# Optimization experiments

Measured on AMD Instinct MI355X. Metric: run time of the kernel, lower is better.

The kernel has to match this reference:

```python
import jax, jax.numpy as jnp
import numpy as np

N_LEVELS = 16
F_PER_LEVEL = 2
T = 1 << 19  # hashmap size per level
BASE_RES = 16
DST_RES = 4096
B = float(np.exp(np.log(DST_RES / BASE_RES) / (N_LEVELS - 1)))  # per-level scale
MOVING_STEP = 1.0 / 4096.0
AABB_MIN = -1.5
AABB_MAX = 1.5
GEO_FEAT_DIM = 15
CORNERS = np.array([[i, j, k] for i in (0, 1) for j in (0, 1) for k in (0, 1)], dtype=np.int32)  # [8,3]
PRIMES = np.array([1, 2654435761, 805459861], dtype=np.uint32)


def mlp(h, Ws):
    # tcnn FullyFusedMLP: bias-free linear layers, ReLU hidden, linear output
    for W in Ws[:-1]:
        h = jax.nn.relu(h @ W)
    return h @ Ws[-1]


def freq_encode(x, n_freqs):
    # tcnn Frequency encoding: sin/cos(2^f * pi * x) per dim/freq; [N,D] -> [N, D*n_freqs*2]
    f = (2.0 ** jnp.arange(n_freqs, dtype=jnp.float32)) * jnp.pi
    xf = x[..., None] * f  # [N, D, nf]
    return jnp.concatenate([jnp.sin(xf), jnp.cos(xf)], axis=-1).reshape(x.shape[0], -1)


def sh_encode_deg4(d):
    # real spherical harmonics, degree 4 (16 coeffs), unit direction input
    x, y, z = d[..., 0], d[..., 1], d[..., 2]
    xy, yz, xz = x * y, y * z, x * z
    x2, y2, z2 = x * x, y * y, z * z
    return jnp.stack([
        0.28209479177387814 * jnp.ones_like(x),
        -0.48860251190291987 * y,
        0.48860251190291987 * z,
        -0.48860251190291987 * x,
        1.0925484305920792 * xy,
        -1.0925484305920792 * yz,
        0.94617469575755997 * z2 - 0.31539156525251999,
        -1.0925484305920792 * xz,
        0.54627421529603959 * (x2 - y2),
        0.59004358992664352 * y * (y2 - 3.0 * x2),
        2.8906114426405538 * xy * z,
        0.45704579946446572 * y * (1.0 - 5.0 * z2),
        0.3731763325901154 * z * (5.0 * z2 - 3.0),
        0.45704579946446572 * x * (1.0 - 5.0 * z2),
        1.4453057213202769 * z * (x2 - y2),
        0.59004358992664352 * x * (3.0 * y2 - x2),
    ], axis=-1)  # [N,16]


def hash_encode(x, tables):
    # x: [N,3] in [0,1]; tables: [L, T, F]. Multi-res grid w/ trilinear interp;
    # dense indexing for small levels, spatial hashing for large ones (tcnn semantics).
    outs = []
    for l in range(N_LEVELS):
        scale = BASE_RES * (B ** l) - 1.0
        res = int(np.ceil(scale)) + 1
        pos = x * scale + 0.5
        pos0 = jnp.floor(pos)
        frac = pos - pos0
        c = pos0.astype(jnp.int32)[:, None, :] + CORNERS[None]  # [N,8,3]
        if res ** 3 <= T:
            idx = c[..., 0] + res * (c[..., 1] + res * c[..., 2])
        else:
            cu = c.astype(jnp.uint32)
            idx = (cu[..., 0] * PRIMES[0]) ^ (cu[..., 1] * PRIMES[1]) ^ (cu[..., 2] * PRIMES[2])
            idx = (idx % np.uint32(T)).astype(jnp.int32)
        feats = tables[l][idx]  # [N,8,F] gather
        w = jnp.prod(jnp.where(CORNERS[None] == 1, frac[:, None, :], 1.0 - frac[:, None, :]), axis=-1)  # [N,8]
        outs.append(jnp.einsum('ncf,nc->nf', feats, w))
    return jnp.concatenate(outs, axis=-1)  # [N, L*F]


def _w(k, fan_in, fan_out):
    return jax.random.normal(k, (fan_in, fan_out), jnp.float32) / np.sqrt(fan_in)


def setup_inputs() -> dict:
    key = jax.random.key(0)
    ks = jax.random.split(key, 12)
    N = 524288
    positions = jax.random.uniform(ks[0], (N, 3), jnp.float32, -1.2, 1.2)
    t = jax.random.uniform(ks[1], (N, 1), jnp.float32)
    directions = jax.random.normal(ks[2], (N, 3), jnp.float32)
    tables = jax.random.uniform(ks[3], (N_LEVELS, T, F_PER_LEVEL), jnp.float32, -1e-4, 1e-4)
    return {
        'positions': positions, 't': t, 'directions': directions, 'tables': tables,
        'w_wrap0': _w(ks[4], 32, 64), 'w_wrap1': _w(ks[5], 64, 64), 'w_wrap2': _w(ks[6], 64, 3),
        'w_base0': _w(ks[7], 32, 64), 'w_base1': _w(ks[8], 64, 1 + GEO_FEAT_DIM),
        'w_head0': _w(ks[9], 16 + GEO_FEAT_DIM, 64), 'w_head1': _w(ks[10], 64, 64), 'w_head2': _w(ks[11], 64, 3),
    }


def reference(positions, t, directions, tables,
              w_wrap0, w_wrap1, w_wrap2, w_base0, w_base1,
              w_head0, w_head1, w_head2):
    # query_move: frequency-encode (x,t), tiny MLP -> offsets, scaled by MOVING_STEP
    enc = freq_encode(jnp.concatenate([positions, t], axis=-1), 4)  # [N,32]
    offsets = mlp(enc, [w_wrap0, w_wrap1, w_wrap2])  # [N,3]
    x_move = positions + offsets * MOVING_STEP
    # normalize to aabb unit cube
    xn = (x_move - AABB_MIN) / (AABB_MAX - AABB_MIN)
    selector = jnp.all((xn > 0.0) & (xn < 1.0), axis=-1)
    hash_feat = hash_encode(xn, tables)  # [N,32]
    base = mlp(hash_feat, [w_base0, w_base1])  # [N,16]
    density = jnp.exp(base[:, :1] - 1.0) * selector[:, None].astype(base.dtype)  # trunc_exp(x-1)
    geo = base[:, 1:]
    dirs = directions / jnp.linalg.norm(directions, axis=-1, keepdims=True)
    sh = sh_encode_deg4(dirs)  # [N,16]
    rgb = jax.nn.sigmoid(mlp(jnp.concatenate([sh, geo], axis=-1), [w_head0, w_head1, w_head2]))
    return jnp.concatenate([rgb, density], axis=-1)  # [N,4] = (rgb, density)
```

## Files before the change

kernel.cpp:

```cpp
#include <hip/hip_runtime.h>
#include <math.h>

#define TPB   128
#define HTPB  256
#define HPTS  4
#define CHUNK 32
#define LDW   68
constexpr int  N_LVL = 16;
constexpr unsigned TBL = 1u << 19;
constexpr float MOVE_STEP = 1.0f / 4096.0f;

typedef __attribute__((ext_vector_type(8))) short short8;
typedef __attribute__((ext_vector_type(4))) float f32x4;
typedef __attribute__((ext_vector_type(4), aligned(8))) float f32x4u;

struct LevelParams { float scale[N_LVL]; int res[N_LVL]; int dense[N_LVL]; };

enum { C_W0 = 0, C_W1 = 4, C_W2 = 12, C_B0 = 14, C_B1 = 18, C_H0 = 20, C_H1 = 24, C_H2 = 32, C_TOT = 34 };

struct LayerDesc { const float* W; int K; int N; int ksteps; int ntiles; int cbase; };
struct AllLayers { LayerDesc L[8]; };

__device__ __forceinline__ unsigned short f2bf(float x) {
    unsigned int u = __float_as_uint(x);
    u += 0x7FFFu + ((u >> 16) & 1u);
    return (unsigned short)(u >> 16);
}
__device__ __forceinline__ float bf2f(unsigned short h) {
    return __uint_as_float(((unsigned int)h) << 16);
}
__device__ __forceinline__ unsigned pk(unsigned short a, unsigned short b) {
    return (unsigned)a | ((unsigned)b << 16);
}
__device__ __forceinline__ unsigned sel4(uint4 w, unsigned i) {
    const unsigned lo = (i & 1u) ? w.y : w.x;
    const unsigned hi = (i & 1u) ? w.w : w.z;
    return (i & 2u) ? hi : lo;
}

__device__ __forceinline__ unsigned cvt_pk_bf16(float a, float b) {
    unsigned r;
    asm("v_cvt_pk_bf16_f32 %0, %1, %2" : "=v"(r) : "v"(a), "v"(b));
    return r;
}
__device__ __forceinline__ void split_pair(float a, float b, unsigned& hp, unsigned& lp) {
    hp = cvt_pk_bf16(a, b);
    const float ha = __uint_as_float(hp << 16);
    const float hb = __uint_as_float(hp & 0xffff0000u);
    lp = cvt_pk_bf16(a - ha, b - hb);
}

__global__ __launch_bounds__(256) void k_prep(AllLayers al, unsigned short* __restrict__ wfrag)
{
    const LayerDesc d = al.L[blockIdx.x];
    const int total = d.ksteps * d.ntiles * 64;
    for (int slot = threadIdx.x; slot < total; slot += 256) {
        const int lane = slot & 63;
        const int c = slot >> 6;
        const int s = c / d.ntiles;
        const int t = c - s * d.ntiles;
        short8 hv, lv;
#pragma unroll
        for (int j = 0; j < 8; ++j) {
            const int k = s * 32 + ((lane >> 4) << 3) + j;
            const int n = t * 16 + (lane & 15);
            const float w = (k < d.K && n < d.N) ? d.W[k * d.N + n] : 0.f;
            const unsigned short hi = f2bf(w);
            const unsigned short lo = f2bf(w - bf2f(hi));
            hv[j] = (short)hi;
            lv[j] = (short)lo;
        }
        short8* b8 = reinterpret_cast<short8*>(wfrag + (size_t)(d.cbase + c) * 1024);
        b8[lane]      = hv;
        b8[64 + lane] = lv;
    }
}

__global__ __launch_bounds__(256) void k_tab16(
    const float* __restrict__ g_tab, unsigned* __restrict__ tab16,
    int n_dense, int n_hashed)
{
    const size_t total_pairs = (size_t)n_hashed * (TBL / 2);
    const size_t gstride = (size_t)gridDim.x * 256;
    const float* __restrict__ src = g_tab + (size_t)n_dense * (TBL * 2);
    for (size_t i = (size_t)blockIdx.x * 256 + threadIdx.x; i < total_pairs; i += gstride) {
        const f32x4 v = reinterpret_cast<const f32x4*>(src)[i];
        uint2 o;
        o.x = pk(f2bf(v[0]), f2bf(v[1]));
        o.y = pk(f2bf(v[2]), f2bf(v[3]));
        reinterpret_cast<uint2*>(tab16)[i] = o;
    }
}

template<int KSTEPS, int NTILES, int TERMS, bool RELU>
__device__ __forceinline__ void wave_layer(float* X,
                                           const unsigned short* __restrict__ wfrag, int cbase,
                                           int wrow, int lane)
{
    f32x4 acc[2][NTILES];
#pragma unroll
    for (int ms = 0; ms < 2; ++ms)
#pragma unroll
        for (int t = 0; t < NTILES; ++t) acc[ms][t] = f32x4{0.f, 0.f, 0.f, 0.f};
    const int r15 = lane & 15, q = lane >> 4;
    const short8* wf8 = reinterpret_cast<const short8*>(wfrag) + (size_t)cbase * 128;
#pragma unroll
    for (int s = 0; s < KSTEPS; ++s) {
        short8 ah[2], al[2];
#pragma unroll
        for (int ms = 0; ms < 2; ++ms) {
            const float* xp = X + (size_t)(wrow + ms * 16 + r15) * LDW + s * 32 + q * 8;
            const f32x4 x0 = reinterpret_cast<const f32x4*>(xp)[0];
            const f32x4 x1 = reinterpret_cast<const f32x4*>(xp)[1];
            union { unsigned u[4]; short8 s8; } uh, ul;
            if (TERMS == 3) {
                split_pair(x0[0], x0[1], uh.u[0], ul.u[0]);
                split_pair(x0[2], x0[3], uh.u[1], ul.u[1]);
                split_pair(x1[0], x1[1], uh.u[2], ul.u[2]);
                split_pair(x1[2], x1[3], uh.u[3], ul.u[3]);
                al[ms] = ul.s8;
            } else {
                uh.u[0] = cvt_pk_bf16(x0[0], x0[1]);
                uh.u[1] = cvt_pk_bf16(x0[2], x0[3]);
                uh.u[2] = cvt_pk_bf16(x1[0], x1[1]);
                uh.u[3] = cvt_pk_bf16(x1[2], x1[3]);
            }
            ah[ms] = uh.s8;
        }
#pragma unroll
        for (int t = 0; t < NTILES; ++t) {
            const short8* cp = wf8 + (size_t)(s * NTILES + t) * 128;
            const short8 bh = cp[lane];
            short8 bl;
            if (TERMS == 3) bl = cp[64 + lane];
#pragma unroll
            for (int ms = 0; ms < 2; ++ms) {
                acc[ms][t] = __builtin_amdgcn_mfma_f32_16x16x32_bf16(ah[ms], bh, acc[ms][t], 0, 0, 0);
                if (TERMS == 3) {
                    acc[ms][t] = __builtin_amdgcn_mfma_f32_16x16x32_bf16(al[ms], bh, acc[ms][t], 0, 0, 0);
                    acc[ms][t] = __builtin_amdgcn_mfma_f32_16x16x32_bf16(ah[ms], bl, acc[ms][t], 0, 0, 0);
                }
            }
        }
    }
#pragma unroll
    for (int ms = 0; ms < 2; ++ms)
#pragma unroll
        for (int t = 0; t < NTILES; ++t)
#pragma unroll
            for (int r = 0; r < 4; ++r) {
                float v = acc[ms][t][r];
                if (RELU) v = fmaxf(v, 0.f);
                X[(size_t)(wrow + ms * 16 + q * 4 + r) * LDW + t * 16 + r15] = v;
            }
}

__global__ __launch_bounds__(256, 4) void k_warp_mfma(
    const float* __restrict__ g_pos, const float* __restrict__ g_t,
    const float* __restrict__ g_tab,
    const unsigned short* __restrict__ wfrag,
    float* __restrict__ xn4,
    unsigned* __restrict__ featp, size_t stride, int N, int n_dense, LevelParams lp)
{
    __shared__ float buf[128 * LDW];
    const int tid = threadIdx.x;
    const int base = blockIdx.x * 128;
    const int p = tid & 127;
    const int pn = min(base + p, N - 1);
    const float PI_F = 3.14159265358979323846f;

    {
        const int dpair = tid >> 7;
        float v0, v1;
        if (dpair == 0) { v0 = g_pos[3 * pn + 0]; v1 = g_pos[3 * pn + 1]; }
        else            { v0 = g_pos[3 * pn + 2]; v1 = g_t[pn]; }
#pragma unroll
        for (int e = 0; e < 2; ++e) {
            const float x = e ? v1 : v0;
            const int d = dpair * 2 + e;
            f32x4 sv, cv;
#pragma unroll
            for (int k = 0; k < 4; ++k) {
                const float a = x * (PI_F * (float)(1 << k));
                sv[k] = __sinf(a);
                cv[k] = __cosf(a);
            }
            *reinterpret_cast<f32x4*>(&buf[(size_t)p * LDW + d * 8])     = sv;
            *reinterpret_cast<f32x4*>(&buf[(size_t)p * LDW + d * 8 + 4]) = cv;
        }
    }
    __syncthreads();
    const int lane = tid & 63, wrow = (tid >> 6) * 32;
    wave_layer<1, 4, 1, true >(buf, wfrag, C_W0, wrow, lane);
    wave_layer<2, 4, 1, true >(buf, wfrag, C_W1, wrow, lane);
    wave_layer<2, 1, 1, false>(buf, wfrag, C_W2, wrow, lane);

    const int prow = wrow + (lane & 31);
    const int sub  = lane >> 5;
    const int n = base + prow;
    const int pn2 = min(n, N - 1);
    const float ox = buf[(size_t)prow * LDW + 0];
    const float oy = buf[(size_t)prow * LDW + 1];
    const float oz = buf[(size_t)prow * LDW + 2];
    const float xnv[3] = { (g_pos[3 * pn2 + 0] + ox * MOVE_STEP + 1.5f) / 3.0f,
                           (g_pos[3 * pn2 + 1] + oy * MOVE_STEP + 1.5f) / 3.0f,
                           (g_pos[3 * pn2 + 2] + oz * MOVE_STEP + 1.5f) / 3.0f };
    if (sub == 0 && n < N) {
        reinterpret_cast<f32x4*>(xn4)[n] = f32x4{ xnv[0], xnv[1], xnv[2], 0.f };
    }

    const int dmid = min(3, n_dense);
    const int l0 = sub ? dmid : 0;
    const int l1 = sub ? n_dense : dmid;
    for (int l = l0; l < l1; ++l) {
        const float scale = lp.scale[l];
        const int res = lp.res[l];
        float fr[3]; int c0[3];
#pragma unroll
        for (int d = 0; d < 3; ++d) {
            const float pp = xnv[d] * scale + 0.5f;
            const float fl = floorf(pp);
            fr[d] = pp - fl;
            c0[d] = (int)fl;
        }
        const float* __restrict__ tbl = g_tab + (size_t)l * (size_t)(TBL * 2);
        f32x4u v[4];
#pragma unroll
        for (int pc = 0; pc < 4; ++pc) {
            const int cj = pc >> 1, ck = pc & 1;
            const int idx = c0[0] + res * ((c0[1] + cj) + res * (c0[2] + ck));
            v[pc] = *reinterpret_cast<const f32x4u*>(tbl + (size_t)idx * 2);
        }
        float f0 = 0.f, f1 = 0.f;
        const float wx0 = 1.f - fr[0], wx1 = fr[0];
#pragma unroll
        for (int pc = 0; pc < 4; ++pc) {
            const int cj = pc >> 1, ck = pc & 1;
            const float wyz = (cj ? fr[1] : 1.f - fr[1]) * (ck ? fr[2] : 1.f - fr[2]);
            f0 = fmaf(wx0 * wyz, v[pc][0], f0);
            f1 = fmaf(wx0 * wyz, v[pc][1], f1);
            f0 = fmaf(wx1 * wyz, v[pc][2], f0);
            f1 = fmaf(wx1 * wyz, v[pc][3], f1);
        }
        if (n < N) {
            __builtin_nontemporal_store(pk(f2bf(f0), f2bf(f1)), &featp[(size_t)l * stride + n]);
        }
    }
}

__global__ __launch_bounds__(HTPB) void k_hash_all16(
    const unsigned* __restrict__ tab16,
    const float* __restrict__ xn4,
    unsigned* __restrict__ featp, size_t stride, int N, int n_dense, LevelParams lp)
{
    const int l = n_dense + blockIdx.y;
    const float scale = lp.scale[l];
    const unsigned* __restrict__ tbl = tab16 + (size_t)blockIdx.y * TBL;
    unsigned* __restrict__ op = featp + (size_t)l * stride;

    const int base = blockIdx.x * (HTPB * HPTS) + threadIdx.x;

#pragma unroll
    for (int b = 0; b < HPTS; b += 2) {
        int nn[2]; bool av[2];
        f32x4 xs[2];
#pragma unroll
        for (int j = 0; j < 2; ++j) {
            nn[j] = base + (b + j) * HTPB;
            av[j] = nn[j] < N;
            xs[j] = reinterpret_cast<const f32x4*>(xn4)[av[j] ? nn[j] : 0];
        }

        float frx[2];
        float wyz[2][4];
        uint4 w4[2][4];
        unsigned vodd[2][4] = {};
        unsigned a3p[2], mm[2];
        bool far_[2];
#pragma unroll
        for (int j = 0; j < 2; ++j) {
            int c0[3]; float fr[3];
#pragma unroll
            for (int d = 0; d < 3; ++d) {
                const float pp = xs[j][d] * scale + 0.5f;
                const float fl = floorf(pp);
                fr[d] = pp - fl;
                c0[d] = (int)fl;
            }
            frx[j] = fr[0];
            const unsigned ux  = (unsigned)c0[0];
            const unsigned ry0 = (unsigned)c0[1] * 2654435761u;
            const unsigned ry1 = (unsigned)(c0[1] + 1) * 2654435761u;
            const unsigned rz0 = (unsigned)c0[2] * 805459861u;
            const unsigned rz1 = (unsigned)(c0[2] + 1) * 805459861u;
            mm[j]  = ux ^ (ux + 1u);
            far_[j] = mm[j] > 3u;
            const float wy0 = 1.f - fr[1], wy1 = fr[1];
            const float wz0 = 1.f - fr[2], wz1 = fr[2];
            wyz[j][0] = wy0 * wz0; wyz[j][1] = wy0 * wz1;
            wyz[j][2] = wy1 * wz0; wyz[j][3] = wy1 * wz1;
            const unsigned rr[4] = { ry0 ^ rz0, ry0 ^ rz1, ry1 ^ rz0, ry1 ^ rz1 };
            unsigned a3 = 0;
#pragma unroll
            for (int pc = 0; pc < 4; ++pc) {
                const unsigned iA = (ux ^ rr[pc]) & (TBL - 1u);
                a3 |= (iA & 3u) << (2 * pc);
                w4[j][pc] = *reinterpret_cast<const uint4*>(tbl + (iA & ~3u));
            }
            a3p[j] = a3;
            if (far_[j]) {
#pragma unroll
                for (int pc = 0; pc < 4; ++pc) {
                    const unsigned iB = ((ux + 1u) ^ rr[pc]) & (TBL - 1u);
                    vodd[j][pc] = tbl[iB];
                }
            }
        }

#pragma unroll
        for (int j = 0; j < 2; ++j) {
            float f0 = 0.f, f1 = 0.f;
            const float wx0 = 1.f - frx[j], wx1 = frx[j];
#pragma unroll
            for (int pc = 0; pc < 4; ++pc) {
                const unsigned a3 = (a3p[j] >> (2 * pc)) & 3u;
                const unsigned vA = sel4(w4[j][pc], a3);
                const unsigned vB = far_[j] ? vodd[j][pc] : sel4(w4[j][pc], a3 ^ mm[j]);
                const float wA = wx0 * wyz[j][pc];
                const float wB = wx1 * wyz[j][pc];
                f0 = fmaf(wA, bf2f((unsigned short)(vA & 0xffffu)), f0);
                f1 = fmaf(wA, bf2f((unsigned short)(vA >> 16)), f1);
                f0 = fmaf(wB, bf2f((unsigned short)(vB & 0xffffu)), f0);
                f1 = fmaf(wB, bf2f((unsigned short)(vB >> 16)), f1);
            }
            if (av[j]) __builtin_nontemporal_store(pk(f2bf(f0), f2bf(f1)), &op[nn[j]]);
        }
    }
}

__global__ __launch_bounds__(256, 4) void k_final_mfma(
    const unsigned* __restrict__ featp, size_t stride,
    const float* __restrict__ xn4,
    const float* __restrict__ g_dir,
    const unsigned short* __restrict__ wfrag,
    float* __restrict__ g_out, int N)
{
    __shared__ float buf[128 * LDW];
    const int tid = threadIdx.x;
    const int base = blockIdx.x * 128;
    const int p = tid & 127;
    const int pn = min(base + p, N - 1);
    const int g = tid >> 7;

#pragma unroll
    for (int j = 0; j < 8; ++j) {
        const int l = g * 8 + j;
        const unsigned v = __builtin_nontemporal_load(&featp[(size_t)l * stride + pn]);
        buf[(size_t)p * LDW + 2 * l]     = bf2f((unsigned short)(v & 0xffffu));
        buf[(size_t)p * LDW + 2 * l + 1] = bf2f((unsigned short)(v >> 16));
    }
    __syncthreads();

    const int lane = tid & 63, wrow = (tid >> 6) * 32;
    wave_layer<1, 4, 1, true >(buf, wfrag, C_B0, wrow, lane);
    wave_layer<2, 1, 1, false>(buf, wfrag, C_B1, wrow, lane);
    __syncthreads();

    float density = 0.f;
    if (tid < 128) {
        float bb[16];
        const f32x4* bv = reinterpret_cast<const f32x4*>(&buf[(size_t)tid * LDW]);
#pragma unroll
        for (int g4 = 0; g4 < 4; ++g4) {
            const f32x4 v = bv[g4];
#pragma unroll
            for (int j = 0; j < 4; ++j) bb[4 * g4 + j] = v[j];
        }
        const f32x4 xv = reinterpret_cast<const f32x4*>(xn4)[pn];
        const bool sel = xv[0] > 0.f && xv[0] < 1.f && xv[1] > 0.f && xv[1] < 1.f &&
                         xv[2] > 0.f && xv[2] < 1.f;
        density = sel ? expf(bb[0] - 1.0f) : 0.0f;

        const float ddx = g_dir[3 * pn + 0];
        const float ddy = g_dir[3 * pn + 1];
        const float ddz = g_dir[3 * pn + 2];
        const float nrm = sqrtf(ddx * ddx + ddy * ddy + ddz * ddz);
        const float x = ddx / nrm, y = ddy / nrm, z = ddz / nrm;
        const float xy = x * y, yz = y * z, xz = x * z;
        const float x2 = x * x, y2 = y * y, z2 = z * z;
        f32x4 o0, o1, o2, o3, o4, o5, o6, o7;
        o0[0] = 0.28209479177387814f;
        o0[1] = -0.48860251190291987f * y;
        o0[2] = 0.48860251190291987f * z;
        o0[3] = -0.48860251190291987f * x;
        o1[0] = 1.0925484305920792f * xy;
        o1[1] = -1.0925484305920792f * yz;
        o1[2] = 0.94617469575756f * z2 - 0.31539156525252f;
        o1[3] = -1.0925484305920792f * xz;
        o2[0] = 0.5462742152960396f * (x2 - y2);
        o2[1] = 0.5900435899266435f * y * (y2 - 3.0f * x2);
        o2[2] = 2.890611442640554f * xy * z;
        o2[3] = 0.4570457994644657f * y * (1.0f - 5.0f * z2);
        o3[0] = 0.3731763325901154f * z * (5.0f * z2 - 3.0f);
        o3[1] = 0.4570457994644657f * x * (1.0f - 5.0f * z2);
        o3[2] = 1.445305721320277f * z * (x2 - y2);
        o3[3] = 0.5900435899266435f * x * (3.0f * y2 - x2);
        o4[0] = bb[1];  o4[1] = bb[2];  o4[2] = bb[3];  o4[3] = bb[4];
        o5[0] = bb[5];  o5[1] = bb[6];  o5[2] = bb[7];  o5[3] = bb[8];
        o6[0] = bb[9];  o6[1] = bb[10]; o6[2] = bb[11]; o6[3] = bb[12];
        o7[0] = bb[13]; o7[1] = bb[14]; o7[2] = bb[15]; o7[3] = 0.f;
        f32x4* wb = reinterpret_cast<f32x4*>(&buf[(size_t)tid * LDW]);
        wb[0] = o0; wb[1] = o1; wb[2] = o2; wb[3] = o3;
        wb[4] = o4; wb[5] = o5; wb[6] = o6; wb[7] = o7;
    }
    __syncthreads();

    wave_layer<1, 4, 3, true >(buf, wfrag, C_H0, wrow, lane);
    wave_layer<2, 4, 3, true >(buf, wfrag, C_H1, wrow, lane);
    wave_layer<2, 1, 3, false>(buf, wfrag, C_H2, wrow, lane);
    __syncthreads();

    if (tid < 128 && base + tid < N) {
        const int n = base + tid;
        float4 o;
        o.x = 1.0f / (1.0f + expf(-buf[(size_t)tid * LDW + 0]));
        o.y = 1.0f / (1.0f + expf(-buf[(size_t)tid * LDW + 1]));
        o.z = 1.0f / (1.0f + expf(-buf[(size_t)tid * LDW + 2]));
        o.w = density;
        *reinterpret_cast<float4*>(g_out + (size_t)n * 4) = o;
    }
}

template<int IN, int OUT, bool RELU>
__device__ __forceinline__ void layer(const float* __restrict__ W,
                                      const float* __restrict__ hin,
                                      float* __restrict__ A,
                                      float* __restrict__ out)
{
#pragma unroll
    for (int j = 0; j < OUT; ++j) out[j] = 0.f;
#pragma unroll
    for (int c = 0; c < IN; c += CHUNK) {
#pragma unroll
        for (int i = 0; i < CHUNK; ++i) {
            if (c + i < IN) A[i * TPB] = RELU ? fmaxf(hin[c + i], 0.f) : hin[c + i];
        }
        const int cnt = (IN - c < CHUNK) ? (IN - c) : CHUNK;
#pragma unroll 4
        for (int i = 0; i < cnt; ++i) {
            const float a = A[i * TPB];
            const float* __restrict__ Wr = W + (size_t)(c + i) * OUT;
#pragma unroll
            for (int j = 0; j < OUT; ++j)
                out[j] = fmaf(a, Wr[j], out[j]);
        }
    }
}

__global__ __launch_bounds__(TPB, 4) void dngp_mono(
    const float* __restrict__ g_pos, const float* __restrict__ g_t,
    const float* __restrict__ g_dir, const float* __restrict__ g_tab,
    const float* __restrict__ Ww0, const float* __restrict__ Ww1, const float* __restrict__ Ww2,
    const float* __restrict__ Wb0, const float* __restrict__ Wb1,
    const float* __restrict__ Wh0, const float* __restrict__ Wh1, const float* __restrict__ Wh2,
    float* __restrict__ g_out, int N, LevelParams lp)
{
    __shared__ float s_act[CHUNK * TPB];
    const int tid = threadIdx.x;
    const int n = blockIdx.x * TPB + tid;
    if (n >= N) return;
    float* __restrict__ A = s_act + tid;

    const float px = g_pos[3 * n + 0];
    const float py = g_pos[3 * n + 1];
    const float pz = g_pos[3 * n + 2];
    const float tt = g_t[n];

    float enc[32];
    {
        const float xin[4] = { px, py, pz, tt };
        const float PI_F = 3.14159265358979323846f;
#pragma unroll
        for (int d = 0; d < 4; ++d)
#pragma unroll
            for (int k = 0; k < 4; ++k) {
                float s, c;
                sincosf(xin[d] * (PI_F * (float)(1 << k)), &s, &c);
                enc[d * 8 + k]     = s;
                enc[d * 8 + 4 + k] = c;
            }
    }

    float h[64], h2[64], off[3];
    layer<32, 64, false>(Ww0, enc, A, h);
    layer<64, 64, true >(Ww1, h,   A, h2);
    layer<64, 3,  true >(Ww2, h2,  A, off);

    const float xn[3] = { (px + off[0] * MOVE_STEP + 1.5f) / 3.0f,
                          (py + off[1] * MOVE_STEP + 1.5f) / 3.0f,
                          (pz + off[2] * MOVE_STEP + 1.5f) / 3.0f };
    const bool sel = xn[0] > 0.f && xn[0] < 1.f && xn[1] > 0.f && xn[1] < 1.f &&
                     xn[2] > 0.f && xn[2] < 1.f;

    float feat[32];
#pragma unroll 2
    for (int l = 0; l < N_LVL; ++l) {
        const float scale = lp.scale[l];
        const int res = lp.res[l];
        float fr[3]; int c0[3];
#pragma unroll
        for (int d = 0; d < 3; ++d) {
            const float pp = xn[d] * scale + 0.5f;
            const float fl = floorf(pp);
            fr[d] = pp - fl;
            c0[d] = (int)fl;
        }
        const float* __restrict__ tbl = g_tab + (size_t)l * (size_t)(TBL * 2);
        float f0 = 0.f, f1 = 0.f;
        if (lp.dense[l]) {
#pragma unroll
            for (int c = 0; c < 8; ++c) {
                const int ci = (c >> 2) & 1, cj = (c >> 1) & 1, ck = c & 1;
                const unsigned idx = (unsigned)((c0[0] + ci) + res * ((c0[1] + cj) + res * (c0[2] + ck)));
                const float2 f = *reinterpret_cast<const float2*>(tbl + (size_t)idx * 2);
                const float w = (ci ? fr[0] : 1.f - fr[0]) * (cj ? fr[1] : 1.f - fr[1]) * (ck ? fr[2] : 1.f - fr[2]);
                f0 = fmaf(w, f.x, f0);
                f1 = fmaf(w, f.y, f1);
            }
        } else {
#pragma unroll
            for (int c = 0; c < 8; ++c) {
                const int ci = (c >> 2) & 1, cj = (c >> 1) & 1, ck = c & 1;
                const unsigned hx = (unsigned)(c0[0] + ci);
                const unsigned hy = (unsigned)(c0[1] + cj) * 2654435761u;
                const unsigned hz = (unsigned)(c0[2] + ck) * 805459861u;
                const unsigned idx = (hx ^ hy ^ hz) & (TBL - 1u);
                const float2 f = *reinterpret_cast<const float2*>(tbl + (size_t)idx * 2);
                const float w = (ci ? fr[0] : 1.f - fr[0]) * (cj ? fr[1] : 1.f - fr[1]) * (ck ? fr[2] : 1.f - fr[2]);
                f0 = fmaf(w, f.x, f0);
                f1 = fmaf(w, f.y, f1);
            }
        }
        feat[2 * l]     = f0;
        feat[2 * l + 1] = f1;
    }

    layer<32, 64, false>(Wb0, feat, A, h);
    float b[16];
    layer<64, 16, true >(Wb1, h, A, b);
    const float density = sel ? expf(b[0] - 1.0f) : 0.0f;

    float hin[31];
    {
        const float ddx = g_dir[3 * n + 0];
        const float ddy = g_dir[3 * n + 1];
        const float ddz = g_dir[3 * n + 2];
        const float nrm = sqrtf(ddx * ddx + ddy * ddy + ddz * ddz);
        const float x = ddx / nrm, y = ddy / nrm, z = ddz / nrm;
        const float xy = x * y, yz = y * z, xz = x * z;
        const float x2_ = x * x, y2 = y * y, z2 = z * z;
        hin[0]  = 0.28209479177387814f;
        hin[1]  = -0.48860251190291987f * y;
        hin[2]  = 0.48860251190291987f * z;
        hin[3]  = -0.48860251190291987f * x;
        hin[4]  = 1.0925484305920792f * xy;
        hin[5]  = -1.0925484305920792f * yz;
        hin[6]  = 0.94617469575756f * z2 - 0.31539156525252f;
        hin[7]  = -1.0925484305920792f * xz;
        hin[8]  = 0.5462742152960396f * (x2_ - y2);
        hin[9]  = 0.5900435899266435f * y * (y2 - 3.0f * x2_);
        hin[10] = 2.890611442640554f * xy * z;
        hin[11] = 0.4570457994644657f * y * (1.0f - 5.0f * z2);
        hin[12] = 0.3731763325901154f * z * (5.0f * z2 - 3.0f);
        hin[13] = 0.4570457994644657f * x * (1.0f - 5.0f * z2);
        hin[14] = 1.445305721320277f * z * (x2_ - y2);
        hin[15] = 0.5900435899266435f * x * (3.0f * y2 - x2_);
#pragma unroll
        for (int j = 0; j < 15; ++j) hin[16 + j] = b[1 + j];
    }

    layer<31, 64, false>(Wh0, hin, A, h);
    layer<64, 64, true >(Wh1, h,   A, h2);
    float rgb[3];
    layer<64, 3,  true >(Wh2, h2,  A, rgb);

    float4 o;
    o.x = 1.0f / (1.0f + expf(-rgb[0]));
    o.y = 1.0f / (1.0f + expf(-rgb[1]));
    o.z = 1.0f / (1.0f + expf(-rgb[2]));
    o.w = density;
    *reinterpret_cast<float4*>(g_out + (size_t)n * 4) = o;
}

extern "C" void kernel_launch(void* const* d_in, const int* in_sizes, int n_in,
                              void* d_out, int out_size, void* d_ws, size_t ws_size,
                              hipStream_t stream)
{
    const float* g_pos = (const float*)d_in[0];
    const float* g_t   = (const float*)d_in[1];
    const float* g_dir = (const float*)d_in[2];
    const float* g_tab = (const float*)d_in[3];
    const float* Ww0   = (const float*)d_in[4];
    const float* Ww1   = (const float*)d_in[5];
    const float* Ww2   = (const float*)d_in[6];
    const float* Wb0   = (const float*)d_in[7];
    const float* Wb1   = (const float*)d_in[8];
    const float* Wh0   = (const float*)d_in[9];
    const float* Wh1   = (const float*)d_in[10];
    const float* Wh2   = (const float*)d_in[11];
    const int N = in_sizes[0] / 3;

    LevelParams lp;
    int n_dense = 0;
    const double Bv = exp(log(4096.0 / 16.0) / 15.0);
    for (int l = 0; l < N_LVL; ++l) {
        const double s = 16.0 * pow(Bv, (double)l) - 1.0;
        lp.scale[l] = (float)s;
        const int r = (int)ceil(s) + 1;
        lp.res[l] = r;
        lp.dense[l] = ((long long)r * r * r <= (long long)TBL) ? 1 : 0;
        if (lp.dense[l]) n_dense = l + 1;
    }
    const int n_hashed = N_LVL - n_dense;

    const size_t stride = ((size_t)N + 259) & ~(size_t)3;
    const size_t ws_need = (size_t)C_TOT * 2048
                         + stride * 4 * 4
                         + stride * 4 * 16
                         + (size_t)n_hashed * TBL * 4;

    if (ws_size >= ws_need) {
        unsigned short* wfrag = (unsigned short*)d_ws;
        float* xn4 = (float*)((char*)d_ws + (size_t)C_TOT * 2048);
        unsigned* featp = (unsigned*)(xn4 + 4 * stride);
        unsigned* tab16 = featp + 16 * stride;

        AllLayers al;
        al.L[0] = { Ww0, 32, 64, 1, 4, C_W0 };
        al.L[1] = { Ww1, 64, 64, 2, 4, C_W1 };
        al.L[2] = { Ww2, 64,  3, 2, 1, C_W2 };
        al.L[3] = { Wb0, 32, 64, 1, 4, C_B0 };
        al.L[4] = { Wb1, 64, 16, 2, 1, C_B1 };
        al.L[5] = { Wh0, 31, 64, 1, 4, C_H0 };
        al.L[6] = { Wh1, 64, 64, 2, 4, C_H1 };
        al.L[7] = { Wh2, 64,  3, 2, 1, C_H2 };

        const int nchunk = (N + HTPB * HPTS - 1) / (HTPB * HPTS);

        dim3 mgrid((N + 127) / 128), mblock(256);
        dim3 hgrid(nchunk, n_hashed), hblock(HTPB);

        hipLaunchKernelGGL(k_prep, dim3(8), dim3(256), 0, stream, al, wfrag);
        hipLaunchKernelGGL(k_tab16, dim3(2048), dim3(256), 0, stream,
                           g_tab, tab16, n_dense, n_hashed);

        hipLaunchKernelGGL(k_warp_mfma, mgrid, mblock, 0, stream,
                           g_pos, g_t, g_tab, wfrag, xn4,
                           featp, stride, N, n_dense, lp);

        hipLaunchKernelGGL(k_hash_all16, hgrid, hblock, 0, stream,
                           tab16, xn4, featp, stride, N, n_dense, lp);

        hipLaunchKernelGGL(k_final_mfma, mgrid, mblock, 0, stream,
                           featp, stride, xn4, g_dir,
                           wfrag, (float*)d_out, N);
    } else {
        dim3 grid((N + TPB - 1) / TPB), block(TPB);
        hipLaunchKernelGGL(dngp_mono, grid, block, 0, stream,
                           g_pos, g_t, g_dir, g_tab,
                           Ww0, Ww1, Ww2, Wb0, Wb1, Wh0, Wh1, Wh2,
                           (float*)d_out, N, lp);
    }
}
```

Measured before the change: 238.5 us.

## Fuse hashed-level gathers into final MLP kernel, drop separate hash kernel

Removes the standalone hashed-level gather kernel and performs those table lookups inside the final MLP kernel, writing interpolated features straight into shared memory instead of round-tripping them through global bf16 feature planes. Normalized positions are staged in shared memory and reused for the selector check. This saves one launch and the global write/read of the hashed features. In exchange, the level-major gather ordering across the whole grid, which kept each level's table hot in cache, is lost, and gather latency now sits in a kernel constrained to 4 blocks per CU with large LDS use.

```diff
diff --git a/kernel.cpp b/kernel.cpp
--- a/kernel.cpp
+++ b/kernel.cpp
@@ -3,7 +3,6 @@
 
 #define TPB   128
 #define HTPB  256
-#define HPTS  4
 #define CHUNK 32
 #define LDW   68
 constexpr int  N_LVL = 16;
@@ -37,7 +36,6 @@
     const unsigned hi = (i & 1u) ? w.w : w.z;
     return (i & 2u) ? hi : lo;
 }
-
 __device__ __forceinline__ unsigned cvt_pk_bf16(float a, float b) {
     unsigned r;
     asm("v_cvt_pk_bf16_f32 %0, %1, %2" : "=v"(r) : "v"(a), "v"(b));
@@ -48,6 +46,61 @@
     const float ha = __uint_as_float(hp << 16);
     const float hb = __uint_as_float(hp & 0xffff0000u);
     lp = cvt_pk_bf16(a - ha, b - hb);
+}
+
+__device__ __forceinline__ void hash_gather(const unsigned* __restrict__ tbl, float scale,
+                                            const float xnv0, const float xnv1, const float xnv2,
+                                            float& f0, float& f1)
+{
+    const float xn[3] = { xnv0, xnv1, xnv2 };
+    int c0[3]; float fr[3];
+#pragma unroll
+    for (int d = 0; d < 3; ++d) {
+        const float pp = xn[d] * scale + 0.5f;
+        const float fl = floorf(pp);
+        fr[d] = pp - fl;
+        c0[d] = (int)fl;
+    }
+    const unsigned ux  = (unsigned)c0[0];
+    const unsigned ry0 = (unsigned)c0[1] * 2654435761u;
+    const unsigned ry1 = (unsigned)(c0[1] + 1) * 2654435761u;
+    const unsigned rz0 = (unsigned)c0[2] * 805459861u;
+    const unsigned rz1 = (unsigned)(c0[2] + 1) * 805459861u;
+    const unsigned mm = ux ^ (ux + 1u);
+    const bool far_ = mm > 3u;
+    const float wy0 = 1.f - fr[1], wy1 = fr[1];
+    const float wz0 = 1.f - fr[2], wz1 = fr[2];
+    const float wyz[4] = { wy0 * wz0, wy0 * wz1, wy1 * wz0, wy1 * wz1 };
+    const unsigned rr[4] = { ry0 ^ rz0, ry0 ^ rz1, ry1 ^ rz0, ry1 ^ rz1 };
+    uint4 w4[4]; unsigned a3 = 0;
+#pragma unroll
+    for (int pc = 0; pc < 4; ++pc) {
+        const unsigned iA = (ux ^ rr[pc]) & (TBL - 1u);
+        a3 |= (iA & 3u) << (2 * pc);
+        w4[pc] = *reinterpret_cast<const uint4*>(tbl + (iA & ~3u));
+    }
+    unsigned vodd[4] = {};
+    if (far_) {
+#pragma unroll
+        for (int pc = 0; pc < 4; ++pc) {
+            const unsigned iB = ((ux + 1u) ^ rr[pc]) & (TBL - 1u);
+            vodd[pc] = tbl[iB];
+        }
+    }
+    f0 = 0.f; f1 = 0.f;
+    const float wx0 = 1.f - fr[0], wx1 = fr[0];
+#pragma unroll
+    for (int pc = 0; pc < 4; ++pc) {
+        const unsigned a3p = (a3 >> (2 * pc)) & 3u;
+        const unsigned vA = sel4(w4[pc], a3p);
+        const unsigned vB = far_ ? vodd[pc] : sel4(w4[pc], a3p ^ mm);
+        const float wA = wx0 * wyz[pc];
+        const float wB = wx1 * wyz[pc];
+        f0 = fmaf(wA, bf2f((unsigned short)(vA & 0xffffu)), f0);
+        f1 = fmaf(wA, bf2f((unsigned short)(vA >> 16)), f1);
+        f0 = fmaf(wB, bf2f((unsigned short)(vB & 0xffffu)), f0);
+        f1 = fmaf(wB, bf2f((unsigned short)(vB >> 16)), f1);
+    }
 }
 
 __global__ __launch_bounds__(256) void k_prep(AllLayers al, unsigned short* __restrict__ wfrag)
@@ -248,102 +301,13 @@
     }
 }
 
-__global__ __launch_bounds__(HTPB) void k_hash_all16(
-    const unsigned* __restrict__ tab16,
-    const float* __restrict__ xn4,
-    unsigned* __restrict__ featp, size_t stride, int N, int n_dense, LevelParams lp)
-{
-    const int l = n_dense + blockIdx.y;
-    const float scale = lp.scale[l];
-    const unsigned* __restrict__ tbl = tab16 + (size_t)blockIdx.y * TBL;
-    unsigned* __restrict__ op = featp + (size_t)l * stride;
-
-    const int base = blockIdx.x * (HTPB * HPTS) + threadIdx.x;
-
-#pragma unroll
-    for (int b = 0; b < HPTS; b += 2) {
-        int nn[2]; bool av[2];
-        f32x4 xs[2];
-#pragma unroll
-        for (int j = 0; j < 2; ++j) {
-            nn[j] = base + (b + j) * HTPB;
-            av[j] = nn[j] < N;
-            xs[j] = reinterpret_cast<const f32x4*>(xn4)[av[j] ? nn[j] : 0];
-        }
-
-        float frx[2];
-        float wyz[2][4];
-        uint4 w4[2][4];
-        unsigned vodd[2][4] = {};
-        unsigned a3p[2], mm[2];
-        bool far_[2];
-#pragma unroll
-        for (int j = 0; j < 2; ++j) {
-            int c0[3]; float fr[3];
-#pragma unroll
-            for (int d = 0; d < 3; ++d) {
-                const float pp = xs[j][d] * scale + 0.5f;
-                const float fl = floorf(pp);
-                fr[d] = pp - fl;
-                c0[d] = (int)fl;
-            }
-            frx[j] = fr[0];
-            const unsigned ux  = (unsigned)c0[0];
-            const unsigned ry0 = (unsigned)c0[1] * 2654435761u;
-            const unsigned ry1 = (unsigned)(c0[1] + 1) * 2654435761u;
-            const unsigned rz0 = (unsigned)c0[2] * 805459861u;
-            const unsigned rz1 = (unsigned)(c0[2] + 1) * 805459861u;
-            mm[j]  = ux ^ (ux + 1u);
-            far_[j] = mm[j] > 3u;
-            const float wy0 = 1.f - fr[1], wy1 = fr[1];
-            const float wz0 = 1.f - fr[2], wz1 = fr[2];
-            wyz[j][0] = wy0 * wz0; wyz[j][1] = wy0 * wz1;
-            wyz[j][2] = wy1 * wz0; wyz[j][3] = wy1 * wz1;
-            const unsigned rr[4] = { ry0 ^ rz0, ry0 ^ rz1, ry1 ^ rz0, ry1 ^ rz1 };
-            unsigned a3 = 0;
-#pragma unroll
-            for (int pc = 0; pc < 4; ++pc) {
-                const unsigned iA = (ux ^ rr[pc]) & (TBL - 1u);
-                a3 |= (iA & 3u) << (2 * pc);
-                w4[j][pc] = *reinterpret_cast<const uint4*>(tbl + (iA & ~3u));
-            }
-            a3p[j] = a3;
-            if (far_[j]) {
-#pragma unroll
-                for (int pc = 0; pc < 4; ++pc) {
-                    const unsigned iB = ((ux + 1u) ^ rr[pc]) & (TBL - 1u);
-                    vodd[j][pc] = tbl[iB];
-                }
-            }
-        }
-
-#pragma unroll
-        for (int j = 0; j < 2; ++j) {
-            float f0 = 0.f, f1 = 0.f;
-            const float wx0 = 1.f - frx[j], wx1 = frx[j];
-#pragma unroll
-            for (int pc = 0; pc < 4; ++pc) {
-                const unsigned a3 = (a3p[j] >> (2 * pc)) & 3u;
-                const unsigned vA = sel4(w4[j][pc], a3);
-                const unsigned vB = far_[j] ? vodd[j][pc] : sel4(w4[j][pc], a3 ^ mm[j]);
-                const float wA = wx0 * wyz[j][pc];
-                const float wB = wx1 * wyz[j][pc];
-                f0 = fmaf(wA, bf2f((unsigned short)(vA & 0xffffu)), f0);
-                f1 = fmaf(wA, bf2f((unsigned short)(vA >> 16)), f1);
-                f0 = fmaf(wB, bf2f((unsigned short)(vB & 0xffffu)), f0);
-                f1 = fmaf(wB, bf2f((unsigned short)(vB >> 16)), f1);
-            }
-            if (av[j]) __builtin_nontemporal_store(pk(f2bf(f0), f2bf(f1)), &op[nn[j]]);
-        }
-    }
-}
-
-__global__ __launch_bounds__(256, 4) void k_final_mfma(
+__global__ __launch_bounds__(256, 4) void k_final_fused(
     const unsigned* __restrict__ featp, size_t stride,
     const float* __restrict__ xn4,
+    const unsigned* __restrict__ tab16,
     const float* __restrict__ g_dir,
     const unsigned short* __restrict__ wfrag,
-    float* __restrict__ g_out, int N)
+    float* __restrict__ g_out, int N, int n_dense, LevelParams lp)
 {
     __shared__ float buf[128 * LDW];
     const int tid = threadIdx.x;
@@ -352,12 +316,39 @@
     const int pn = min(base + p, N - 1);
     const int g = tid >> 7;
 
-#pragma unroll
-    for (int j = 0; j < 8; ++j) {
-        const int l = g * 8 + j;
-        const unsigned v = __builtin_nontemporal_load(&featp[(size_t)l * stride + pn]);
-        buf[(size_t)p * LDW + 2 * l]     = bf2f((unsigned short)(v & 0xffffu));
-        buf[(size_t)p * LDW + 2 * l + 1] = bf2f((unsigned short)(v >> 16));
+    if (g == 0) {
+        const f32x4 xv = reinterpret_cast<const f32x4*>(xn4)[pn];
+        buf[(size_t)p * LDW + 64] = xv[0];
+        buf[(size_t)p * LDW + 65] = xv[1];
+        buf[(size_t)p * LDW + 66] = xv[2];
+        for (int j = 0; j < min(3, n_dense); ++j) {
+            const unsigned v = __builtin_nontemporal_load(&featp[(size_t)j * stride + pn]);
+            buf[(size_t)p * LDW + 2 * j]     = bf2f((unsigned short)(v & 0xffffu));
+            buf[(size_t)p * LDW + 2 * j + 1] = bf2f((unsigned short)(v >> 16));
+        }
+    } else {
+        for (int j = min(3, n_dense); j < n_dense; ++j) {
+            const unsigned v = __builtin_nontemporal_load(&featp[(size_t)j * stride + pn]);
+            buf[(size_t)p * LDW + 2 * j]     = bf2f((unsigned short)(v & 0xffffu));
+            buf[(size_t)p * LDW + 2 * j + 1] = bf2f((unsigned short)(v >> 16));
+        }
+    }
+    __syncthreads();
+
+    {
+        const int nh = N_LVL - n_dense;
+        const int tot = 128 * nh;
+        for (int i = tid; i < tot; i += 256) {
+            const int pp = i & 127;
+            const int li = i >> 7;
+            const int l = n_dense + li;
+            const float x0 = buf[(size_t)pp * LDW + 64];
+            const float x1 = buf[(size_t)pp * LDW + 65];
+            const float x2 = buf[(size_t)pp * LDW + 66];
+            float f0, f1;
+            hash_gather(tab16 + (size_t)li * TBL, lp.scale[l], x0, x1, x2, f0, f1);
+            *reinterpret_cast<float2*>(&buf[(size_t)pp * LDW + 2 * l]) = float2{ f0, f1 };
+        }
     }
     __syncthreads();
 
@@ -376,9 +367,11 @@
 #pragma unroll
             for (int j = 0; j < 4; ++j) bb[4 * g4 + j] = v[j];
         }
-        const f32x4 xv = reinterpret_cast<const f32x4*>(xn4)[pn];
-        const bool sel = xv[0] > 0.f && xv[0] < 1.f && xv[1] > 0.f && xv[1] < 1.f &&
-                         xv[2] > 0.f && xv[2] < 1.f;
+        const float x0v = buf[(size_t)tid * LDW + 64];
+        const float x1v = buf[(size_t)tid * LDW + 65];
+        const float x2v = buf[(size_t)tid * LDW + 66];
+        const bool sel = x0v > 0.f && x0v < 1.f && x1v > 0.f && x1v < 1.f &&
+                         x2v > 0.f && x2v < 1.f;
         density = sel ? expf(bb[0] - 1.0f) : 0.0f;
 
         const float ddx = g_dir[3 * pn + 0];
@@ -645,10 +638,7 @@
         al.L[6] = { Wh1, 64, 64, 2, 4, C_H1 };
         al.L[7] = { Wh2, 64,  3, 2, 1, C_H2 };
 
-        const int nchunk = (N + HTPB * HPTS - 1) / (HTPB * HPTS);
-
         dim3 mgrid((N + 127) / 128), mblock(256);
-        dim3 hgrid(nchunk, n_hashed), hblock(HTPB);
 
         hipLaunchKernelGGL(k_prep, dim3(8), dim3(256), 0, stream, al, wfrag);
         hipLaunchKernelGGL(k_tab16, dim3(2048), dim3(256), 0, stream,
@@ -658,12 +648,9 @@
                            g_pos, g_t, g_tab, wfrag, xn4,
                            featp, stride, N, n_dense, lp);
 
-        hipLaunchKernelGGL(k_hash_all16, hgrid, hblock, 0, stream,
-                           tab16, xn4, featp, stride, N, n_dense, lp);
-
-        hipLaunchKernelGGL(k_final_mfma, mgrid, mblock, 0, stream,
-                           featp, stride, xn4, g_dir,
-                           wfrag, (float*)d_out, N);
+        hipLaunchKernelGGL(k_final_fused, mgrid, mblock, 0, stream,
+                           featp, stride, xn4, tab16, g_dir,
+                           wfrag, (float*)d_out, N, n_dense, lp);
     } else {
         dim3 grid((N + TPB - 1) / TPB), block(TPB);
         hipLaunchKernelGGL(dngp_mono, grid, block, 0, stream,
```

After: 351.9 us. 1.48x slower.
